# Performance work log

Measured on AMD Instinct MI355X. Metric: run time of the kernel, lower is better.

Reference implementation:

```python
import jax, jax.numpy as jnp
import numpy as np

MODEL_DIM = 1024
RANK = 128

def setup_inputs() -> dict:
    key = jax.random.key(0)
    k1, k2 = jax.random.split(key)
    batch = jax.random.normal(k1, (8, 512, MODEL_DIM), dtype=jnp.float32)
    # nn.init.uniform_(proj, -0.05, 0.05)
    proj = jax.random.uniform(k2, (MODEL_DIM, RANK), dtype=jnp.float32, minval=-0.05, maxval=0.05)
    return {"batch": batch, "proj": proj}

def reference(batch, proj):
    # project: (B, S, D) @ (D, R) -> (B, S, R)
    transformed = jnp.matmul(batch, proj)
    # all-pairs squared L2 distance via broadcast diff, matching the torch math
    # diffs: (B, S, S, R)
    diffs = transformed[:, :, None, :] - transformed[:, None, :, :]
    squared_distances = jnp.sum(diffs * diffs, axis=-1)  # (B, S, S)
    return squared_distances
```

## Files before the change

kernel.cpp:

```cpp
#include <hip/hip_runtime.h>

#define SEQ 512
#define MD  1024
#define RK  128

typedef __attribute__((ext_vector_type(8))) short  bf16x8;
typedef __attribute__((ext_vector_type(4))) float  floatx4;
typedef __attribute__((ext_vector_type(4))) unsigned int uint4v;
typedef __attribute__((ext_vector_type(4))) unsigned short ushortx4;

__device__ inline unsigned short f2bf(float f) {
    union { float f; unsigned u; } v; v.f = f;
    unsigned r = v.u + 0x7fffu + ((v.u >> 16) & 1u);
    return (unsigned short)(r >> 16);
}
__device__ inline float bf2f(unsigned short s) {
    union { unsigned u; float f; } v; v.u = ((unsigned)s) << 16;
    return v.f;
}

__global__ __launch_bounds__(256) void transpose_proj(
    const float* __restrict__ proj, unsigned short* __restrict__ Pt)
{
    __shared__ float Ls[64 * 132];
    const int t  = threadIdx.x;
    const int k0 = blockIdx.x * 64;

    {
        int kr = t >> 2;
        int nb = (t & 3) * 32;
        #pragma unroll
        for (int cc = 0; cc < 8; ++cc) {
            float4 v = *(const float4*)(proj + (size_t)(k0 + kr) * RK + nb + cc * 4);
            *(float4*)(Ls + kr * 132 + nb + cc * 4) = v;
        }
    }
    __syncthreads();
    {
        int n  = t >> 1;
        int kh = (t & 1) * 32;
        unsigned short tmp[32];
        #pragma unroll
        for (int kk = 0; kk < 32; ++kk)
            tmp[kk] = f2bf(Ls[(kh + kk) * 132 + n]);
        #pragma unroll
        for (int q = 0; q < 4; ++q)
            *(uint4v*)(Pt + (size_t)n * MD + k0 + kh + q * 8) = *(uint4v*)(tmp + q * 8);
    }
}

__global__ __launch_bounds__(512) void proj_mfma(
    const float* __restrict__ batch, const unsigned short* __restrict__ Pt,
    unsigned short* __restrict__ T)
{
    __shared__ float Red[8 * 2048];

    const int t    = threadIdx.x;
    const int w    = t >> 6;
    const int l    = t & 63;
    const int lm   = l & 15;
    const int quad = l >> 4;
    const int r0   = blockIdx.x * 16;

    floatx4 acc[8];
    #pragma unroll
    for (int i = 0; i < 8; ++i) acc[i] = (floatx4){0.f, 0.f, 0.f, 0.f};

    const float* arow = batch + (size_t)(r0 + lm) * MD + w * 128 + quad * 8;

    #pragma unroll
    for (int s = 0; s < 4; ++s) {
        float4 a0 = *(const float4*)(arow + s * 32);
        float4 a1 = *(const float4*)(arow + s * 32 + 4);
        bf16x8 av;
        av[0] = (short)f2bf(a0.x); av[1] = (short)f2bf(a0.y);
        av[2] = (short)f2bf(a0.z); av[3] = (short)f2bf(a0.w);
        av[4] = (short)f2bf(a1.x); av[5] = (short)f2bf(a1.y);
        av[6] = (short)f2bf(a1.z); av[7] = (short)f2bf(a1.w);
        #pragma unroll
        for (int nt = 0; nt < 8; ++nt) {
            bf16x8 bv = *(const bf16x8*)(Pt + (size_t)(nt * 16 + lm) * MD
                                         + w * 128 + s * 32 + quad * 8);
            acc[nt] = __builtin_amdgcn_mfma_f32_16x16x32_bf16(av, bv, acc[nt], 0, 0, 0);
        }
    }

    #pragma unroll
    for (int nt = 0; nt < 8; ++nt) {
        #pragma unroll
        for (int r = 0; r < 4; ++r) {
            int elem = (quad * 4 + r) * 128 + nt * 16 + lm;
            Red[w * 2048 + elem] = acc[nt][r];
        }
    }
    __syncthreads();

    {
        unsigned short tmp[4];
        #pragma unroll
        for (int i = 0; i < 4; ++i) {
            int e = t * 4 + i;
            float s = 0.f;
            #pragma unroll
            for (int ww = 0; ww < 8; ++ww) s += Red[ww * 2048 + e];
            tmp[i] = f2bf(s);
        }
        *(ushortx4*)(T + (size_t)r0 * RK + t * 4) = *(ushortx4*)tmp;
    }
}

#define LDB 136

__global__ __launch_bounds__(256) void dist_mfma(
    const unsigned short* __restrict__ T, float* __restrict__ out)
{
    __shared__ unsigned short Ti[64 * LDB];
    __shared__ unsigned short Tj[64 * LDB];
    __shared__ float nI[64], nJ[64];

    const int t    = threadIdx.x;
    const int w    = t >> 6;
    const int l    = t & 63;
    const int lm   = l & 15;
    const int quad = l >> 4;
    const int jt = blockIdx.x, it = blockIdx.y, b = blockIdx.z;
    const int i0 = it * 64, j0 = jt * 64;
    const unsigned short* Tb = T + (size_t)b * SEQ * RK;

    {
        int row = t >> 2, kq = (t & 3) * 32;
        const unsigned short* si = Tb + (size_t)(i0 + row) * RK + kq;
        const unsigned short* sj = Tb + (size_t)(j0 + row) * RK + kq;
        #pragma unroll
        for (int q = 0; q < 4; ++q) {
            *(uint4v*)(Ti + row * LDB + kq + q * 8) = *(const uint4v*)(si + q * 8);
            *(uint4v*)(Tj + row * LDB + kq + q * 8) = *(const uint4v*)(sj + q * 8);
        }
    }
    __syncthreads();

    if (t < 64) {
        float s = 0.f;
        #pragma unroll
        for (int k8 = 0; k8 < 16; ++k8) {
            bf16x8 v = *(const bf16x8*)(Ti + t * LDB + k8 * 8);
            #pragma unroll
            for (int j = 0; j < 8; ++j) {
                float f = bf2f((unsigned short)v[j]); s += f * f;
            }
        }
        nI[t] = s;
    } else if (t < 128) {
        int r = t - 64;
        float s = 0.f;
        #pragma unroll
        for (int k8 = 0; k8 < 16; ++k8) {
            bf16x8 v = *(const bf16x8*)(Tj + r * LDB + k8 * 8);
            #pragma unroll
            for (int j = 0; j < 8; ++j) {
                float f = bf2f((unsigned short)v[j]); s += f * f;
            }
        }
        nJ[r] = s;
    }
    __syncthreads();

    floatx4 acc[4];
    #pragma unroll
    for (int i = 0; i < 4; ++i) acc[i] = (floatx4){0.f, 0.f, 0.f, 0.f};

    #pragma unroll
    for (int s = 0; s < 4; ++s) {
        bf16x8 av = *(const bf16x8*)(Ti + (w * 16 + lm) * LDB + s * 32 + quad * 8);
        #pragma unroll
        for (int nt = 0; nt < 4; ++nt) {
            bf16x8 bv = *(const bf16x8*)(Tj + (nt * 16 + lm) * LDB + s * 32 + quad * 8);
            acc[nt] = __builtin_amdgcn_mfma_f32_16x16x32_bf16(av, bv, acc[nt], 0, 0, 0);
        }
    }

    float niv[4];
    #pragma unroll
    for (int r = 0; r < 4; ++r) niv[r] = nI[w * 16 + quad * 4 + r];

    float* ob = out + ((size_t)b * SEQ + (i0 + w * 16)) * SEQ + j0;
    #pragma unroll
    for (int nt = 0; nt < 4; ++nt) {
        float njv = nJ[nt * 16 + lm];
        #pragma unroll
        for (int r = 0; r < 4; ++r) {
            ob[(size_t)(quad * 4 + r) * SEQ + nt * 16 + lm] =
                niv[r] + njv - 2.f * acc[nt][r];
        }
    }
}

extern "C" void kernel_launch(void* const* d_in, const int* in_sizes, int n_in,
                              void* d_out, int out_size, void* d_ws, size_t ws_size,
                              hipStream_t stream) {
    const float* batch = (const float*)d_in[0];
    const float* proj  = (const float*)d_in[1];
    float* out = (float*)d_out;

    unsigned short* T  = (unsigned short*)d_ws;
    unsigned short* Pt = (unsigned short*)((char*)d_ws + (1 << 20));

    transpose_proj<<<16, 256, 0, stream>>>(proj, Pt);
    proj_mfma<<<256, 512, 0, stream>>>(batch, Pt, T);
    dist_mfma<<<dim3(8, 8, 8), 256, 0, stream>>>(T, out);
}
```

Baseline: 80.79 us.

## Compute row norms in projection kernel and drop per-tile norm recomputation

The projection kernel now computes each row's squared norm from the fp32 sums, reduces it with a wavefront shuffle, and writes it to a workspace buffer. The distance kernel loads these norms instead of recomputing them from shared memory, which removes a serial phase and one barrier. The reduction layout is padded and vectorised, and the proj transpose is split over twice as many blocks. Norms now come from unrounded fp32 values rather than bf16, a small numeric change.

```diff
diff --git a/kernel.cpp b/kernel.cpp
--- a/kernel.cpp
+++ b/kernel.cpp
@@ -14,46 +14,44 @@
     unsigned r = v.u + 0x7fffu + ((v.u >> 16) & 1u);
     return (unsigned short)(r >> 16);
 }
-__device__ inline float bf2f(unsigned short s) {
-    union { unsigned u; float f; } v; v.u = ((unsigned)s) << 16;
-    return v.f;
-}
 
 __global__ __launch_bounds__(256) void transpose_proj(
     const float* __restrict__ proj, unsigned short* __restrict__ Pt)
 {
-    __shared__ float Ls[64 * 132];
+    __shared__ float Ls[64 * 68];
     const int t  = threadIdx.x;
-    const int k0 = blockIdx.x * 64;
+    const int k0 = (blockIdx.x >> 1) * 64;
+    const int n0 = (blockIdx.x & 1) * 64;
 
     {
         int kr = t >> 2;
-        int nb = (t & 3) * 32;
+        int nc = (t & 3) * 16;
         #pragma unroll
-        for (int cc = 0; cc < 8; ++cc) {
-            float4 v = *(const float4*)(proj + (size_t)(k0 + kr) * RK + nb + cc * 4);
-            *(float4*)(Ls + kr * 132 + nb + cc * 4) = v;
+        for (int c = 0; c < 4; ++c) {
+            float4 v = *(const float4*)(proj + (size_t)(k0 + kr) * RK + n0 + nc + c * 4);
+            *(float4*)(Ls + kr * 68 + nc + c * 4) = v;
         }
     }
     __syncthreads();
     {
-        int n  = t >> 1;
-        int kh = (t & 1) * 32;
-        unsigned short tmp[32];
+        int nl = t >> 2;
+        int kh = (t & 3) * 16;
+        unsigned short tmp[16];
         #pragma unroll
-        for (int kk = 0; kk < 32; ++kk)
-            tmp[kk] = f2bf(Ls[(kh + kk) * 132 + n]);
-        #pragma unroll
-        for (int q = 0; q < 4; ++q)
-            *(uint4v*)(Pt + (size_t)n * MD + k0 + kh + q * 8) = *(uint4v*)(tmp + q * 8);
+        for (int kk = 0; kk < 16; ++kk)
+            tmp[kk] = f2bf(Ls[(kh + kk) * 68 + nl]);
+        *(uint4v*)(Pt + (size_t)(n0 + nl) * MD + k0 + kh)     = *(uint4v*)(tmp);
+        *(uint4v*)(Pt + (size_t)(n0 + nl) * MD + k0 + kh + 8) = *(uint4v*)(tmp + 8);
     }
 }
 
+#define REDW 2112
+
 __global__ __launch_bounds__(512) void proj_mfma(
     const float* __restrict__ batch, const unsigned short* __restrict__ Pt,
-    unsigned short* __restrict__ T)
+    unsigned short* __restrict__ T, float* __restrict__ Nrm)
 {
-    __shared__ float Red[8 * 2048];
+    __shared__ float Red[8 * REDW];
 
     const int t    = threadIdx.x;
     const int w    = t >> 6;
@@ -89,30 +87,40 @@
     for (int nt = 0; nt < 8; ++nt) {
         #pragma unroll
         for (int r = 0; r < 4; ++r) {
-            int elem = (quad * 4 + r) * 128 + nt * 16 + lm;
-            Red[w * 2048 + elem] = acc[nt][r];
+            Red[w * REDW + (quad * 4 + r) * 132 + nt * 16 + lm] = acc[nt][r];
         }
     }
     __syncthreads();
 
     {
+        const int row  = t >> 5;
+        const int col4 = (t & 31) * 4;
+        float4 s4 = {0.f, 0.f, 0.f, 0.f};
+        #pragma unroll
+        for (int ww = 0; ww < 8; ++ww) {
+            float4 p = *(const float4*)(Red + ww * REDW + row * 132 + col4);
+            s4.x += p.x; s4.y += p.y; s4.z += p.z; s4.w += p.w;
+        }
         unsigned short tmp[4];
-        #pragma unroll
-        for (int i = 0; i < 4; ++i) {
-            int e = t * 4 + i;
-            float s = 0.f;
-            #pragma unroll
-            for (int ww = 0; ww < 8; ++ww) s += Red[ww * 2048 + e];
-            tmp[i] = f2bf(s);
-        }
-        *(ushortx4*)(T + (size_t)r0 * RK + t * 4) = *(ushortx4*)tmp;
+        tmp[0] = f2bf(s4.x); tmp[1] = f2bf(s4.y);
+        tmp[2] = f2bf(s4.z); tmp[3] = f2bf(s4.w);
+        *(ushortx4*)(T + (size_t)(r0 + row) * RK + col4) = *(ushortx4*)tmp;
+
+        float ss = s4.x * s4.x + s4.y * s4.y + s4.z * s4.z + s4.w * s4.w;
+        ss += __shfl_xor(ss, 1,  64);
+        ss += __shfl_xor(ss, 2,  64);
+        ss += __shfl_xor(ss, 4,  64);
+        ss += __shfl_xor(ss, 8,  64);
+        ss += __shfl_xor(ss, 16, 64);
+        if ((t & 31) == 0) Nrm[r0 + row] = ss;
     }
 }
 
 #define LDB 136
 
 __global__ __launch_bounds__(256) void dist_mfma(
-    const unsigned short* __restrict__ T, float* __restrict__ out)
+    const unsigned short* __restrict__ T, const float* __restrict__ Nrm,
+    float* __restrict__ out)
 {
     __shared__ unsigned short Ti[64 * LDB];
     __shared__ unsigned short Tj[64 * LDB];
@@ -136,32 +144,8 @@
             *(uint4v*)(Ti + row * LDB + kq + q * 8) = *(const uint4v*)(si + q * 8);
             *(uint4v*)(Tj + row * LDB + kq + q * 8) = *(const uint4v*)(sj + q * 8);
         }
-    }
-    __syncthreads();
-
-    if (t < 64) {
-        float s = 0.f;
-        #pragma unroll
-        for (int k8 = 0; k8 < 16; ++k8) {
-            bf16x8 v = *(const bf16x8*)(Ti + t * LDB + k8 * 8);
-            #pragma unroll
-            for (int j = 0; j < 8; ++j) {
-                float f = bf2f((unsigned short)v[j]); s += f * f;
-            }
-        }
-        nI[t] = s;
-    } else if (t < 128) {
-        int r = t - 64;
-        float s = 0.f;
-        #pragma unroll
-        for (int k8 = 0; k8 < 16; ++k8) {
-            bf16x8 v = *(const bf16x8*)(Tj + r * LDB + k8 * 8);
-            #pragma unroll
-            for (int j = 0; j < 8; ++j) {
-                float f = bf2f((unsigned short)v[j]); s += f * f;
-            }
-        }
-        nJ[r] = s;
+        if (t < 64)                nI[t]      = Nrm[(size_t)b * SEQ + i0 + t];
+        else if (t < 128)          nJ[t - 64] = Nrm[(size_t)b * SEQ + j0 + (t - 64)];
     }
     __syncthreads();
 
@@ -202,10 +186,11 @@
     const float* proj  = (const float*)d_in[1];
     float* out = (float*)d_out;
 
-    unsigned short* T  = (unsigned short*)d_ws;
-    unsigned short* Pt = (unsigned short*)((char*)d_ws + (1 << 20));
+    unsigned short* T   = (unsigned short*)d_ws;
+    unsigned short* Pt  = (unsigned short*)((char*)d_ws + (1 << 20));
+    float*          Nrm = (float*)((char*)d_ws + (1 << 20) + (1 << 18));
 
-    transpose_proj<<<16, 256, 0, stream>>>(proj, Pt);
-    proj_mfma<<<256, 512, 0, stream>>>(batch, Pt, T);
-    dist_mfma<<<dim3(8, 8, 8), 256, 0, stream>>>(T, out);
+    transpose_proj<<<32, 256, 0, stream>>>(proj, Pt);
+    proj_mfma<<<256, 512, 0, stream>>>(batch, Pt, T, Nrm);
+    dist_mfma<<<dim3(8, 8, 8), 256, 0, stream>>>(T, Nrm, out);
 }
```

After: 79.58 us. About the same (-1.5%).
